# Optimization experiments

Measured on AMD Instinct MI355X. Metric: run time of the kernel, lower is better.

Reference implementation:

```python
import jax, jax.numpy as jnp
import numpy as np

EMBED_DIM = 1024
NUM_HEADS = 16
HEAD_DIM = EMBED_DIM // NUM_HEADS
N, SEQ = 4, 2048


def setup_inputs() -> dict:
    key = jax.random.key(0)
    ks = jax.random.split(key, 9)
    s = 0.02
    return {
        "keys": jax.random.normal(ks[0], (N, SEQ, EMBED_DIM), jnp.float32),
        "values": jax.random.normal(ks[1], (N, SEQ, EMBED_DIM), jnp.float32),
        "queries": jax.random.normal(ks[2], (N, SEQ, EMBED_DIM), jnp.float32),
        "mask": jax.random.randint(ks[3], (N, 1, SEQ, SEQ), 0, 2, jnp.int32),
        "Wk": jax.random.normal(ks[4], (HEAD_DIM, HEAD_DIM), jnp.float32) * s,
        "Wv": jax.random.normal(ks[5], (HEAD_DIM, HEAD_DIM), jnp.float32) * s,
        "Wq": jax.random.normal(ks[6], (HEAD_DIM, HEAD_DIM), jnp.float32) * s,
        "Wo": jax.random.normal(ks[7], (EMBED_DIM, EMBED_DIM), jnp.float32) * s,
        "bo": jax.random.normal(ks[8], (EMBED_DIM,), jnp.float32) * s,
    }


def reference(keys, values, queries, mask, Wk, Wv, Wq, Wo, bo):
    n, key_len, _ = keys.shape
    value_len = values.shape[1]
    query_len = queries.shape[1]
    # Faithful to source: direct reshape (N, L, E) -> (N, H, L, D), no transpose.
    k = keys.reshape(n, NUM_HEADS, key_len, HEAD_DIM) @ Wk.T
    v = values.reshape(n, NUM_HEADS, value_len, HEAD_DIM) @ Wv.T
    q = queries.reshape(n, NUM_HEADS, query_len, HEAD_DIM) @ Wq.T
    # Scaled by sqrt(embed_dim) as in the original (not sqrt(head_dim)).
    energy = jnp.einsum('nhqd,nhkd->nhqk', q, k) / jnp.sqrt(jnp.float32(EMBED_DIM))
    energy = jnp.where(mask == 0, jnp.float32(-1e20), energy)
    attention = jax.nn.softmax(energy, axis=-1)
    att_out = jnp.einsum('nhql,nhld->nhqd', attention, v)
    att_out = att_out.reshape(n, query_len, NUM_HEADS * HEAD_DIM)
    return att_out @ Wo.T + bo
```

## Files before the change

### kernel.cpp

```cpp
#include <hip/hip_runtime.h>

#define SEQ 2048
#define HDIM 64
#define NH 16

typedef __bf16 bf16x8 __attribute__((ext_vector_type(8)));
typedef float f32x4 __attribute__((ext_vector_type(4)));
typedef unsigned short u16x8 __attribute__((ext_vector_type(8)));
typedef unsigned short u16x4 __attribute__((ext_vector_type(4)));
typedef unsigned long long u64;

__device__ __forceinline__ unsigned short f2bf(float f) {
  unsigned int u = __builtin_bit_cast(unsigned int, f);
  u = (u + 0x7FFFu + ((u >> 16) & 1u)) >> 16;
  return (unsigned short)u;
}

__device__ __forceinline__ bf16x8 cvt8(f32x4 a, f32x4 b) {
  u16x8 u;
  u[0] = f2bf(a[0]); u[1] = f2bf(a[1]); u[2] = f2bf(a[2]); u[3] = f2bf(a[3]);
  u[4] = f2bf(b[0]); u[5] = f2bf(b[1]); u[6] = f2bf(b[2]); u[7] = f2bf(b[3]);
  return __builtin_bit_cast(bf16x8, u);
}

__device__ __forceinline__ f32x4 mfma16(bf16x8 a, bf16x8 b, f32x4 c) {
  return __builtin_amdgcn_mfma_f32_16x16x32_bf16(a, b, c, 0, 0, 0);
}

#define QSCALE 0.045084220027780106f

__global__ __launch_bounds__(256) void qkv_proj(
    const float* __restrict__ keys, const float* __restrict__ values,
    const float* __restrict__ queries,
    const float* __restrict__ Wk, const float* __restrict__ Wv,
    const float* __restrict__ Wq,
    unsigned short* __restrict__ kb, unsigned short* __restrict__ vb,
    unsigned short* __restrict__ qb)
{
  const int which = blockIdx.y;
  const float* __restrict__ in = (which == 0) ? keys : (which == 1) ? values : queries;
  const float* __restrict__ W  = (which == 0) ? Wk   : (which == 1) ? Wv     : Wq;
  unsigned short* __restrict__ op = (which == 0) ? kb : (which == 1) ? vb : qb;
  const float osc = (which == 2) ? QSCALE : 1.0f;

  const int tid = threadIdx.x;
  const int w = tid >> 6, lane = tid & 63, c = lane & 15, quad = lane >> 4;

  bf16x8 bw[4][2];
  #pragma unroll
  for (int nt = 0; nt < 4; ++nt)
    #pragma unroll
    for (int hh = 0; hh < 2; ++hh) {
      const float* wr = W + (nt * 16 + c) * 64 + hh * 32 + quad * 8;
      bw[nt][hh] = cvt8(*(const f32x4*)wr, *(const f32x4*)(wr + 4));
    }

  const int m00 = blockIdx.x * 256 + w * 64;
  #pragma unroll
  for (int s = 0; s < 4; ++s) {
    const int m0 = m00 + s * 16;
    const float* xr = in + (size_t)(m0 + c) * 64;
    bf16x8 a0 = cvt8(*(const f32x4*)(xr + quad * 8), *(const f32x4*)(xr + quad * 8 + 4));
    bf16x8 a1 = cvt8(*(const f32x4*)(xr + 32 + quad * 8), *(const f32x4*)(xr + 36 + quad * 8));
    f32x4 acc[4] = {};
    #pragma unroll
    for (int nt = 0; nt < 4; ++nt) {
      acc[nt] = mfma16(a0, bw[nt][0], acc[nt]);
      acc[nt] = mfma16(a1, bw[nt][1], acc[nt]);
    }
    #pragma unroll
    for (int nt = 0; nt < 4; ++nt)
      #pragma unroll
      for (int r = 0; r < 4; ++r)
        op[(size_t)(m0 + quad * 4 + r) * 64 + nt * 16 + c] = f2bf(acc[nt][r] * osc);
  }
}

__global__ __launch_bounds__(256) void cvt_wo(const float* __restrict__ src,
                                              unsigned short* __restrict__ dst)
{
  int i = (blockIdx.x * 256 + threadIdx.x) * 4;
  f32x4 v = *reinterpret_cast<const f32x4*>(src + i);
  u16x4 o;
  o[0] = f2bf(v[0]); o[1] = f2bf(v[1]); o[2] = f2bf(v[2]); o[3] = f2bf(v[3]);
  *reinterpret_cast<u16x4*>(dst + i) = o;
}

__global__ __launch_bounds__(256) void maskpack(const int* __restrict__ mask,
                                                u64* __restrict__ bits)
{
  const int wid = blockIdx.x * 4 + (threadIdx.x >> 6);
  const int lane = threadIdx.x & 63;
  const int* src = mask + (size_t)wid * 1024 + lane;
  u64* dst = bits + (size_t)wid * 16;
  #pragma unroll
  for (int i = 0; i < 16; ++i) {
    u64 b = __ballot(src[i * 64] != 0);
    if (lane == 0) dst[i] = b;
  }
}

__global__ __launch_bounds__(256, 4) void attn2(
    const unsigned short* __restrict__ qb, const unsigned short* __restrict__ kb,
    const unsigned short* __restrict__ vb, const u64* __restrict__ mbits,
    unsigned short* __restrict__ att)
{
  __shared__ __attribute__((aligned(16))) unsigned short Kl[64][72];
  __shared__ __attribute__((aligned(16))) unsigned short Vt[64][72];
  __shared__ __attribute__((aligned(16))) unsigned short Pl[8][16][72];

  const int tid = threadIdx.x;
  const int w = tid >> 6, lane = tid & 63, c = lane & 15, quad = lane >> 4;
  const int h = blockIdx.y, n = blockIdx.z;
  const int q0 = blockIdx.x * 128;
  const size_t hb = (size_t)(n * NH + h) * (SEQ * HDIM);

  bf16x8 aq[2][2];
  #pragma unroll
  for (int qt = 0; qt < 2; ++qt) {
    const unsigned short* qr = qb + hb + (size_t)(q0 + qt * 64 + w * 16 + c) * HDIM;
    aq[qt][0] = *reinterpret_cast<const bf16x8*>(qr + quad * 8);
    aq[qt][1] = *reinterpret_cast<const bf16x8*>(qr + 32 + quad * 8);
  }

  f32x4 o[2][4] = {};
  float ps[2][4] = {};

  const u64* mb = mbits + ((size_t)n * SEQ + q0 + w * 16 + quad * 4) * 32;

  const int krow = tid >> 1, kcol = (tid & 1) * 32;
  const int vlg = tid & 15, vdg = (tid >> 4) & 7;

  for (int k0 = 0; k0 < SEQ; k0 += 64) {
    const int step = k0 >> 6;
    __syncthreads();
    if (tid < 128) {
      const unsigned short* s = kb + hb + (size_t)(k0 + krow) * HDIM + kcol;
      u16x8 x0 = *(const u16x8*)(s);
      u16x8 x1 = *(const u16x8*)(s + 8);
      u16x8 x2 = *(const u16x8*)(s + 16);
      u16x8 x3 = *(const u16x8*)(s + 24);
      *(u16x8*)&Kl[krow][kcol]      = x0;
      *(u16x8*)&Kl[krow][kcol + 8]  = x1;
      *(u16x8*)&Kl[krow][kcol + 16] = x2;
      *(u16x8*)&Kl[krow][kcol + 24] = x3;
    } else {
      const unsigned short* s = vb + hb + (size_t)(k0 + vlg) * HDIM + vdg * 8;
      u16x8 r0 = *(const u16x8*)(s);
      u16x8 r1 = *(const u16x8*)(s + 16 * HDIM);
      u16x8 r2 = *(const u16x8*)(s + 32 * HDIM);
      u16x8 r3 = *(const u16x8*)(s + 48 * HDIM);
      #pragma unroll
      for (int j = 0; j < 8; ++j) {
        u16x4 pk = { r0[j], r1[j], r2[j], r3[j] };
        *(u16x4*)&Vt[vdg * 8 + j][vlg * 4] = pk;
      }
    }
    __syncthreads();

    f32x4 e[2][4] = {};
    #pragma unroll
    for (int t = 0; t < 4; ++t) {
      bf16x8 bk0 = *reinterpret_cast<const bf16x8*>(&Kl[t * 16 + c][quad * 8]);
      bf16x8 bk1 = *reinterpret_cast<const bf16x8*>(&Kl[t * 16 + c][32 + quad * 8]);
      #pragma unroll
      for (int qt = 0; qt < 2; ++qt) {
        e[qt][t] = mfma16(aq[qt][0], bk0, e[qt][t]);
        e[qt][t] = mfma16(aq[qt][1], bk1, e[qt][t]);
      }
    }

    #pragma unroll
    for (int qt = 0; qt < 2; ++qt) {
      #pragma unroll
      for (int r = 0; r < 4; ++r) {
        u64 bits = mb[(size_t)(qt * 64 + r) * 32 + step];
        unsigned int lo = (unsigned int)(bits >> c);
        unsigned int hi = (unsigned int)(bits >> (32 + c));
        float p0 = (lo & 1u)         ? exp2f(e[qt][0][r]) : 0.0f;
        float p1 = ((lo >> 16) & 1u) ? exp2f(e[qt][1][r]) : 0.0f;
        float p2 = (hi & 1u)         ? exp2f(e[qt][2][r]) : 0.0f;
        float p3 = ((hi >> 16) & 1u) ? exp2f(e[qt][3][r]) : 0.0f;
        ps[qt][r] += (p0 + p1) + (p2 + p3);
        u16x4 pk = { f2bf(p0), f2bf(p1), f2bf(p2), f2bf(p3) };
        *(u16x4*)&Pl[w * 2 + qt][quad * 4 + r][c * 4] = pk;
      }
    }
    __threadfence_block();

    bf16x8 ap[2][2];
    #pragma unroll
    for (int qt = 0; qt < 2; ++qt) {
      ap[qt][0] = *reinterpret_cast<const bf16x8*>(&Pl[w * 2 + qt][c][quad * 8]);
      ap[qt][1] = *reinterpret_cast<const bf16x8*>(&Pl[w * 2 + qt][c][32 + quad * 8]);
    }
    #pragma unroll
    for (int dt = 0; dt < 4; ++dt) {
      bf16x8 bv0 = *reinterpret_cast<const bf16x8*>(&Vt[dt * 16 + c][quad * 8]);
      bf16x8 bv1 = *reinterpret_cast<const bf16x8*>(&Vt[dt * 16 + c][32 + quad * 8]);
      #pragma unroll
      for (int qt = 0; qt < 2; ++qt) {
        o[qt][dt] = mfma16(ap[qt][0], bv0, o[qt][dt]);
        o[qt][dt] = mfma16(ap[qt][1], bv1, o[qt][dt]);
      }
    }
  }

  #pragma unroll
  for (int qt = 0; qt < 2; ++qt)
    #pragma unroll
    for (int r = 0; r < 4; ++r) {
      float s = ps[qt][r];
      s += __shfl_xor(s, 1);
      s += __shfl_xor(s, 2);
      s += __shfl_xor(s, 4);
      s += __shfl_xor(s, 8);
      ps[qt][r] = 1.0f / s;
    }

  unsigned short* ob = att + hb;
  #pragma unroll
  for (int qt = 0; qt < 2; ++qt)
    #pragma unroll
    for (int dt = 0; dt < 4; ++dt)
      #pragma unroll
      for (int r = 0; r < 4; ++r)
        ob[(size_t)(q0 + qt * 64 + w * 16 + quad * 4 + r) * HDIM + dt * 16 + c] =
            f2bf(o[qt][dt][r] * ps[qt][r]);
}

__global__ __launch_bounds__(256) void out_proj2(
    const unsigned short* __restrict__ att, const unsigned short* __restrict__ wob,
    const float* __restrict__ bo, float* __restrict__ out)
{
  __shared__ __attribute__((aligned(16))) unsigned short As[128][72];
  __shared__ __attribute__((aligned(16))) unsigned short Bs[128][72];

  const int nb = blockIdx.x, mbk = blockIdx.y;
  const int tid = threadIdx.x;
  const int w = tid >> 6, lane = tid & 63, c = lane & 15, quad = lane >> 4;
  const int wm = w & 1, wn = w >> 1;
  const int m0 = mbk * 128, n0 = nb * 128;
  const int srow = tid >> 1, scol = (tid & 1) * 32;

  f32x4 acc[4][4] = {};

  for (int k0 = 0; k0 < 1024; k0 += 64) {
    __syncthreads();
    {
      const unsigned short* sa = att + (size_t)(m0 + srow) * 1024 + k0 + scol;
      const unsigned short* sb = wob + (size_t)(n0 + srow) * 1024 + k0 + scol;
      #pragma unroll
      for (int i = 0; i < 4; ++i)
        *(u16x8*)&As[srow][scol + i * 8] = *(const u16x8*)(sa + i * 8);
      #pragma unroll
      for (int i = 0; i < 4; ++i)
        *(u16x8*)&Bs[srow][scol + i * 8] = *(const u16x8*)(sb + i * 8);
    }
    __syncthreads();

    #pragma unroll
    for (int kk = 0; kk < 64; kk += 32) {
      bf16x8 af[4];
      #pragma unroll
      for (int mt = 0; mt < 4; ++mt)
        af[mt] = *reinterpret_cast<const bf16x8*>(&As[wm * 64 + mt * 16 + c][kk + quad * 8]);
      #pragma unroll
      for (int nt = 0; nt < 4; ++nt) {
        bf16x8 bf_ = *reinterpret_cast<const bf16x8*>(&Bs[wn * 64 + nt * 16 + c][kk + quad * 8]);
        #pragma unroll
        for (int mt = 0; mt < 4; ++mt)
          acc[mt][nt] = mfma16(af[mt], bf_, acc[mt][nt]);
      }
    }
  }

  #pragma unroll
  for (int nt = 0; nt < 4; ++nt) {
    const int col = n0 + wn * 64 + nt * 16 + c;
    const float bias = bo[col];
    #pragma unroll
    for (int mt = 0; mt < 4; ++mt)
      #pragma unroll
      for (int r = 0; r < 4; ++r)
        out[(size_t)(m0 + wm * 64 + mt * 16 + quad * 4 + r) * 1024 + col] =
            acc[mt][nt][r] + bias;
  }
}

extern "C" void kernel_launch(void* const* d_in, const int* in_sizes, int n_in,
                              void* d_out, int out_size, void* d_ws, size_t ws_size,
                              hipStream_t stream) {
  const float* keys    = (const float*)d_in[0];
  const float* values  = (const float*)d_in[1];
  const float* queries = (const float*)d_in[2];
  const int*   mask    = (const int*)d_in[3];
  const float* Wk      = (const float*)d_in[4];
  const float* Wv      = (const float*)d_in[5];
  const float* Wq      = (const float*)d_in[6];
  const float* Wo      = (const float*)d_in[7];
  const float* bo      = (const float*)d_in[8];
  float* out = (float*)d_out;

  const size_t T = (size_t)4 * NH * SEQ * HDIM;
  unsigned short* ws  = (unsigned short*)d_ws;
  unsigned short* kb  = ws;
  unsigned short* vb  = kb + T;
  unsigned short* qb  = vb + T;
  unsigned short* att = qb + T;
  unsigned short* wob = att + T;
  u64* mbits = (u64*)(wob + 1024 * 1024);

  qkv_proj<<<dim3(512, 3), 256, 0, stream>>>(keys, values, queries,
                                             Wk, Wv, Wq, kb, vb, qb);
  cvt_wo<<<dim3(1024), 256, 0, stream>>>(Wo, wob);
  maskpack<<<dim3(4096), 256, 0, stream>>>(mask, mbits);
  attn2<<<dim3(16, NH, 4), 256, 0, stream>>>(qb, kb, vb, mbits, att);
  out_proj2<<<dim3(8, 64), 256, 0, stream>>>(att, wob, bo, out);
}
```

Baseline: 418.5 us.

## Keep P in registers via transposed QK^T and fp16 PV MFMA

Computes S^T by swapping the MFMA operands, so each lane's accumulator already matches the B-operand layout of a 16x16x16 f16 MFMA. The probabilities are packed to fp16 in registers and fed straight into the PV product, which removes the per-step shared-memory round trip for P. V is now stored as fp16 by the projection kernel, and the V tile layout and padding change to suit the new fragment reads. The risks are fp16 range and precision for V and P (P values are at most 1) and a different LDS bank-conflict pattern.

Result: faster. 377.8 us (-9.7%).

```diff
diff --git a/kernel.cpp b/kernel.cpp
--- a/kernel.cpp
+++ b/kernel.cpp
@@ -8,6 +8,8 @@
 typedef float f32x4 __attribute__((ext_vector_type(4)));
 typedef unsigned short u16x8 __attribute__((ext_vector_type(8)));
 typedef unsigned short u16x4 __attribute__((ext_vector_type(4)));
+typedef _Float16 f16x4 __attribute__((ext_vector_type(4)));
+typedef unsigned int u32x2 __attribute__((ext_vector_type(2)));
 typedef unsigned long long u64;
 
 __device__ __forceinline__ unsigned short f2bf(float f) {
@@ -25,6 +27,17 @@
 
 __device__ __forceinline__ f32x4 mfma16(bf16x8 a, bf16x8 b, f32x4 c) {
   return __builtin_amdgcn_mfma_f32_16x16x32_bf16(a, b, c, 0, 0, 0);
+}
+__device__ __forceinline__ f32x4 mfma16h(f16x4 a, f16x4 b, f32x4 c) {
+  return __builtin_amdgcn_mfma_f32_16x16x16f16(a, b, c, 0, 0, 0);
+}
+
+__device__ __forceinline__ f16x4 pk4h(float a, float b, float cc, float d) {
+  auto h0 = __builtin_amdgcn_cvt_pkrtz(a, b);
+  auto h1 = __builtin_amdgcn_cvt_pkrtz(cc, d);
+  u32x2 u = { __builtin_bit_cast(unsigned int, h0),
+              __builtin_bit_cast(unsigned int, h1) };
+  return __builtin_bit_cast(f16x4, u);
 }
 
 #define QSCALE 0.045084220027780106f
@@ -42,6 +55,7 @@
   const float* __restrict__ W  = (which == 0) ? Wk   : (which == 1) ? Wv     : Wq;
   unsigned short* __restrict__ op = (which == 0) ? kb : (which == 1) ? vb : qb;
   const float osc = (which == 2) ? QSCALE : 1.0f;
+  const bool asf16 = (which == 1);
 
   const int tid = threadIdx.x;
   const int w = tid >> 6, lane = tid & 63, c = lane & 15, quad = lane >> 4;
@@ -71,8 +85,12 @@
     #pragma unroll
     for (int nt = 0; nt < 4; ++nt)
       #pragma unroll
-      for (int r = 0; r < 4; ++r)
-        op[(size_t)(m0 + quad * 4 + r) * 64 + nt * 16 + c] = f2bf(acc[nt][r] * osc);
+      for (int r = 0; r < 4; ++r) {
+        float v = acc[nt][r] * osc;
+        unsigned short bits = asf16
+            ? __builtin_bit_cast(unsigned short, (_Float16)v) : f2bf(v);
+        op[(size_t)(m0 + quad * 4 + r) * 64 + nt * 16 + c] = bits;
+      }
   }
 }
 
@@ -100,14 +118,13 @@
   }
 }
 
-__global__ __launch_bounds__(256, 4) void attn2(
+__global__ __launch_bounds__(256, 4) void attn3(
     const unsigned short* __restrict__ qb, const unsigned short* __restrict__ kb,
     const unsigned short* __restrict__ vb, const u64* __restrict__ mbits,
     unsigned short* __restrict__ att)
 {
   __shared__ __attribute__((aligned(16))) unsigned short Kl[64][72];
-  __shared__ __attribute__((aligned(16))) unsigned short Vt[64][72];
-  __shared__ __attribute__((aligned(16))) unsigned short Pl[8][16][72];
+  __shared__ __attribute__((aligned(16))) unsigned short Vt[64][76];
 
   const int tid = threadIdx.x;
   const int w = tid >> 6, lane = tid & 63, c = lane & 15, quad = lane >> 4;
@@ -124,36 +141,31 @@
   }
 
   f32x4 o[2][4] = {};
-  float ps[2][4] = {};
-
-  const u64* mb = mbits + ((size_t)n * SEQ + q0 + w * 16 + quad * 4) * 32;
+  f32x4 psv[2] = {};
+
+  const u64* mb = mbits + ((size_t)n * SEQ + q0 + w * 16 + c) * 32;
 
   const int krow = tid >> 1, kcol = (tid & 1) * 32;
-  const int vlg = tid & 15, vdg = (tid >> 4) & 7;
+  const int vg = (tid >> 3) & 15, vd8 = tid & 7;
 
   for (int k0 = 0; k0 < SEQ; k0 += 64) {
     const int step = k0 >> 6;
     __syncthreads();
     if (tid < 128) {
       const unsigned short* s = kb + hb + (size_t)(k0 + krow) * HDIM + kcol;
-      u16x8 x0 = *(const u16x8*)(s);
-      u16x8 x1 = *(const u16x8*)(s + 8);
-      u16x8 x2 = *(const u16x8*)(s + 16);
-      u16x8 x3 = *(const u16x8*)(s + 24);
-      *(u16x8*)&Kl[krow][kcol]      = x0;
-      *(u16x8*)&Kl[krow][kcol + 8]  = x1;
-      *(u16x8*)&Kl[krow][kcol + 16] = x2;
-      *(u16x8*)&Kl[krow][kcol + 24] = x3;
+      #pragma unroll
+      for (int i = 0; i < 4; ++i)
+        *(u16x8*)&Kl[krow][kcol + i * 8] = *(const u16x8*)(s + i * 8);
     } else {
-      const unsigned short* s = vb + hb + (size_t)(k0 + vlg) * HDIM + vdg * 8;
+      const unsigned short* s = vb + hb + (size_t)(k0 + vg * 4) * HDIM + vd8 * 8;
       u16x8 r0 = *(const u16x8*)(s);
-      u16x8 r1 = *(const u16x8*)(s + 16 * HDIM);
-      u16x8 r2 = *(const u16x8*)(s + 32 * HDIM);
-      u16x8 r3 = *(const u16x8*)(s + 48 * HDIM);
+      u16x8 r1 = *(const u16x8*)(s + HDIM);
+      u16x8 r2 = *(const u16x8*)(s + 2 * HDIM);
+      u16x8 r3 = *(const u16x8*)(s + 3 * HDIM);
       #pragma unroll
       for (int j = 0; j < 8; ++j) {
         u16x4 pk = { r0[j], r1[j], r2[j], r3[j] };
-        *(u16x4*)&Vt[vdg * 8 + j][vlg * 4] = pk;
+        *(u16x4*)&Vt[vd8 * 8 + j][vg * 4] = pk;
       }
     }
     __syncthreads();
@@ -161,72 +173,63 @@
     f32x4 e[2][4] = {};
     #pragma unroll
     for (int t = 0; t < 4; ++t) {
-      bf16x8 bk0 = *reinterpret_cast<const bf16x8*>(&Kl[t * 16 + c][quad * 8]);
-      bf16x8 bk1 = *reinterpret_cast<const bf16x8*>(&Kl[t * 16 + c][32 + quad * 8]);
+      bf16x8 kf0 = *reinterpret_cast<const bf16x8*>(&Kl[t * 16 + c][quad * 8]);
+      bf16x8 kf1 = *reinterpret_cast<const bf16x8*>(&Kl[t * 16 + c][32 + quad * 8]);
       #pragma unroll
       for (int qt = 0; qt < 2; ++qt) {
-        e[qt][t] = mfma16(aq[qt][0], bk0, e[qt][t]);
-        e[qt][t] = mfma16(aq[qt][1], bk1, e[qt][t]);
-      }
-    }
-
+        e[qt][t] = mfma16(kf0, aq[qt][0], e[qt][t]);
+        e[qt][t] = mfma16(kf1, aq[qt][1], e[qt][t]);
+      }
+    }
+
+    f16x4 pf[2][4];
     #pragma unroll
     for (int qt = 0; qt < 2; ++qt) {
-      #pragma unroll
-      for (int r = 0; r < 4; ++r) {
-        u64 bits = mb[(size_t)(qt * 64 + r) * 32 + step];
-        unsigned int lo = (unsigned int)(bits >> c);
-        unsigned int hi = (unsigned int)(bits >> (32 + c));
-        float p0 = (lo & 1u)         ? exp2f(e[qt][0][r]) : 0.0f;
-        float p1 = ((lo >> 16) & 1u) ? exp2f(e[qt][1][r]) : 0.0f;
-        float p2 = (hi & 1u)         ? exp2f(e[qt][2][r]) : 0.0f;
-        float p3 = ((hi >> 16) & 1u) ? exp2f(e[qt][3][r]) : 0.0f;
-        ps[qt][r] += (p0 + p1) + (p2 + p3);
-        u16x4 pk = { f2bf(p0), f2bf(p1), f2bf(p2), f2bf(p3) };
-        *(u16x4*)&Pl[w * 2 + qt][quad * 4 + r][c * 4] = pk;
-      }
-    }
-    __threadfence_block();
-
-    bf16x8 ap[2][2];
-    #pragma unroll
-    for (int qt = 0; qt < 2; ++qt) {
-      ap[qt][0] = *reinterpret_cast<const bf16x8*>(&Pl[w * 2 + qt][c][quad * 8]);
-      ap[qt][1] = *reinterpret_cast<const bf16x8*>(&Pl[w * 2 + qt][c][32 + quad * 8]);
-    }
+      u64 bits = mb[(size_t)qt * 2048 + step] >> (quad * 4);
+      unsigned int lo = (unsigned int)bits;
+      unsigned int hi = (unsigned int)(bits >> 32);
+      #pragma unroll
+      for (int t = 0; t < 4; ++t) {
+        unsigned int b = (t & 2) ? hi : lo;
+        b >>= (t & 1) * 16;
+        f32x4 ev = e[qt][t];
+        float p0 = (b & 1u)        ? exp2f(ev[0]) : 0.0f;
+        float p1 = ((b >> 1) & 1u) ? exp2f(ev[1]) : 0.0f;
+        float p2 = ((b >> 2) & 1u) ? exp2f(ev[2]) : 0.0f;
+        float p3 = ((b >> 3) & 1u) ? exp2f(ev[3]) : 0.0f;
+        f32x4 pv = { p0, p1, p2, p3 };
+        psv[qt] += pv;
+        pf[qt][t] = pk4h(p0, p1, p2, p3);
+      }
+    }
+
     #pragma unroll
     for (int dt = 0; dt < 4; ++dt) {
-      bf16x8 bv0 = *reinterpret_cast<const bf16x8*>(&Vt[dt * 16 + c][quad * 8]);
-      bf16x8 bv1 = *reinterpret_cast<const bf16x8*>(&Vt[dt * 16 + c][32 + quad * 8]);
-      #pragma unroll
-      for (int qt = 0; qt < 2; ++qt) {
-        o[qt][dt] = mfma16(ap[qt][0], bv0, o[qt][dt]);
-        o[qt][dt] = mfma16(ap[qt][1], bv1, o[qt][dt]);
-      }
-    }
-  }
-
-  #pragma unroll
-  for (int qt = 0; qt < 2; ++qt)
-    #pragma unroll
-    for (int r = 0; r < 4; ++r) {
-      float s = ps[qt][r];
-      s += __shfl_xor(s, 1);
-      s += __shfl_xor(s, 2);
-      s += __shfl_xor(s, 4);
-      s += __shfl_xor(s, 8);
-      ps[qt][r] = 1.0f / s;
-    }
-
-  unsigned short* ob = att + hb;
-  #pragma unroll
-  for (int qt = 0; qt < 2; ++qt)
-    #pragma unroll
-    for (int dt = 0; dt < 4; ++dt)
-      #pragma unroll
-      for (int r = 0; r < 4; ++r)
-        ob[(size_t)(q0 + qt * 64 + w * 16 + quad * 4 + r) * HDIM + dt * 16 + c] =
-            f2bf(o[qt][dt][r] * ps[qt][r]);
+      #pragma unroll
+      for (int t = 0; t < 4; ++t) {
+        f16x4 vf = __builtin_bit_cast(f16x4,
+            *(const u16x4*)&Vt[dt * 16 + c][t * 16 + quad * 4]);
+        o[0][dt] = mfma16h(vf, pf[0][t], o[0][dt]);
+        o[1][dt] = mfma16h(vf, pf[1][t], o[1][dt]);
+      }
+    }
+  }
+
+  #pragma unroll
+  for (int qt = 0; qt < 2; ++qt) {
+    float s = (psv[qt][0] + psv[qt][1]) + (psv[qt][2] + psv[qt][3]);
+    s += __shfl_xor(s, 16);
+    s += __shfl_xor(s, 32);
+    float inv = 1.0f / s;
+    unsigned short* orow =
+        att + hb + (size_t)(q0 + qt * 64 + w * 16 + c) * HDIM + quad * 4;
+    #pragma unroll
+    for (int dt = 0; dt < 4; ++dt) {
+      u16x4 pk = { f2bf(o[qt][dt][0] * inv), f2bf(o[qt][dt][1] * inv),
+                   f2bf(o[qt][dt][2] * inv), f2bf(o[qt][dt][3] * inv) };
+      *(u16x4*)(orow + dt * 16) = pk;
+    }
+  }
 }
 
 __global__ __launch_bounds__(256) void out_proj2(
@@ -315,6 +318,6 @@
                                              Wk, Wv, Wq, kb, vb, qb);
   cvt_wo<<<dim3(1024), 256, 0, stream>>>(Wo, wob);
   maskpack<<<dim3(4096), 256, 0, stream>>>(mask, mbits);
-  attn2<<<dim3(16, NH, 4), 256, 0, stream>>>(qb, kb, vb, mbits, att);
+  attn3<<<dim3(16, NH, 4), 256, 0, stream>>>(qb, kb, vb, mbits, att);
   out_proj2<<<dim3(8, 64), 256, 0, stream>>>(att, wob, bo, out);
 }
```
